# Optimization experiments

Hardware: AMD Instinct MI355X
Metric: run time of the kernel (lower is better)

The kernel has to match this reference:

```python
import jax, jax.numpy as jnp
import numpy as np

D_MODEL = 2048
NUM_HEADS = 32
NUM_KV_HEADS = 8
HEAD_DIM = D_MODEL // NUM_HEADS  # 64
GROUP = NUM_HEADS // NUM_KV_HEADS  # 4


def setup_inputs() -> dict:
    key = jax.random.key(0)
    ks = jax.random.split(key, 9)
    s = 1.0 / np.sqrt(D_MODEL)
    kv_dim = NUM_KV_HEADS * HEAD_DIM
    return {
        "x": jax.random.normal(ks[0], (2, 2048, D_MODEL), dtype=jnp.float32),
        "Wq": jax.random.normal(ks[1], (D_MODEL, D_MODEL), dtype=jnp.float32) * s,
        "bq": jnp.zeros((D_MODEL,), dtype=jnp.float32),
        "Wk": jax.random.normal(ks[2], (D_MODEL, kv_dim), dtype=jnp.float32) * s,
        "bk": jnp.zeros((kv_dim,), dtype=jnp.float32),
        "Wv": jax.random.normal(ks[3], (D_MODEL, kv_dim), dtype=jnp.float32) * s,
        "bv": jnp.zeros((kv_dim,), dtype=jnp.float32),
        "Wo": jax.random.normal(ks[4], (D_MODEL, D_MODEL), dtype=jnp.float32) * s,
        "bo": jnp.zeros((D_MODEL,), dtype=jnp.float32),
    }


def reference(x, Wq, bq, Wk, bk, Wv, bv, Wo, bo):
    B, S, _ = x.shape
    # projections
    q = (x @ Wq + bq).reshape(B, S, NUM_HEADS, HEAD_DIM).transpose(0, 2, 1, 3)      # [B,H,S,Dh]
    k = (x @ Wk + bk).reshape(B, S, NUM_KV_HEADS, HEAD_DIM).transpose(0, 2, 1, 3)   # [B,Hkv,S,Dh]
    v = (x @ Wv + bv).reshape(B, S, NUM_KV_HEADS, HEAD_DIM).transpose(0, 2, 1, 3)
    # expand KV heads to match query heads (repeat_interleave along head dim)
    k = jnp.repeat(k, GROUP, axis=1)  # [B,H,S,Dh]
    v = jnp.repeat(v, GROUP, axis=1)
    scale = 1.0 / np.sqrt(HEAD_DIM).astype(np.float32)
    scores = jnp.einsum('bhqd,bhkd->bhqk', q, k) * scale  # [B,H,S,S]
    attn = jax.nn.softmax(scores, axis=-1)
    out = jnp.einsum('bhqk,bhkd->bhqd', attn, v)          # [B,H,S,Dh]
    out = out.transpose(0, 2, 1, 3).reshape(B, S, NUM_HEADS * HEAD_DIM)
    return out @ Wo + bo
```

## Files before the change

kernel.cpp:

```cpp
#include <hip/hip_runtime.h>
#include <stdint.h>

typedef unsigned short u16;
typedef unsigned int u32;
typedef short bf16x8 __attribute__((ext_vector_type(8)));
typedef float f32x4 __attribute__((ext_vector_type(4)));
typedef u32 u32x2 __attribute__((ext_vector_type(2)));

#define GLOAD_LDS16(gptr, lptr)                                                \
  __builtin_amdgcn_global_load_lds(                                            \
      (__attribute__((address_space(1))) void*)(gptr),                         \
      (__attribute__((address_space(3))) void*)(lptr), 16, 0, 0)

#define WAITV4() asm volatile("s_waitcnt vmcnt(4)" ::: "memory")
#define WAITV0() asm volatile("s_waitcnt vmcnt(0)" ::: "memory")

#if __has_builtin(__builtin_amdgcn_exp2f)
#define EXP2F(x) __builtin_amdgcn_exp2f(x)
#else
#define EXP2F(x) exp2f(x)
#endif

__device__ __forceinline__ u16 f2bf(float f) {
  union { float f; uint32_t u; } v; v.f = f;
  return (u16)((v.u + 0x7fffu + ((v.u >> 16) & 1u)) >> 16);
}
__device__ __forceinline__ float bf2f(u16 h) {
  union { uint32_t u; float f; } v; v.u = ((uint32_t)h) << 16;
  return v.f;
}
__device__ __forceinline__ u32 cvt_pk_bf16(float lo, float hi) {
  u32 r;
  asm("v_cvt_pk_bf16_f32 %0, %1, %2" : "=v"(r) : "v"(lo), "v"(hi));
  return r;
}

__global__ void k_conv_bf16(const float* __restrict__ src, u16* __restrict__ dst, int n8) {
  int i = blockIdx.x * blockDim.x + threadIdx.x;
  if (i >= n8) return;
  const float4* s = (const float4*)src + (size_t)i * 2;
  float4 a = s[0], b = s[1];
  uint4 o;
  o.x = (uint32_t)f2bf(a.x) | ((uint32_t)f2bf(a.y) << 16);
  o.y = (uint32_t)f2bf(a.z) | ((uint32_t)f2bf(a.w) << 16);
  o.z = (uint32_t)f2bf(b.x) | ((uint32_t)f2bf(b.y) << 16);
  o.w = (uint32_t)f2bf(b.z) | ((uint32_t)f2bf(b.w) << 16);
  ((uint4*)dst)[i] = o;
}

__global__ void k_transpose_bf16(const float* __restrict__ src, u16* __restrict__ dst,
                                 int R, int C) {
  __shared__ float tile[32][33];
  int cb = blockIdx.x * 32, rb = blockIdx.y * 32;
  int tx = threadIdx.x, ty = threadIdx.y;
#pragma unroll
  for (int j = 0; j < 4; ++j)
    tile[ty + j * 8][tx] = src[(size_t)(rb + ty + j * 8) * C + cb + tx];
  __syncthreads();
#pragma unroll
  for (int j = 0; j < 4; ++j)
    dst[(size_t)(cb + ty + j * 8) * R + rb + tx] = f2bf(tile[tx][ty + j * 8]);
}

__global__ void k_transpose_v(const u16* __restrict__ cqkv, u16* __restrict__ vt) {
  __shared__ u16 tile[32][34];
  int st = blockIdx.x, dt = blockIdx.y, bk = blockIdx.z;
  int b = bk >> 3, kvh = bk & 7;
  int tx = threadIdx.x, ty = threadIdx.y;
  const u16* src = cqkv + (size_t)(b * 2048 + st * 32) * 3072 + 2560 + kvh * 64 + dt * 32;
#pragma unroll
  for (int j = 0; j < 4; ++j)
    tile[ty + j * 8][tx] = src[(size_t)(ty + j * 8) * 3072 + tx];
  __syncthreads();
  u16* dst = vt + ((size_t)(bk * 64 + dt * 32)) * 2048 + st * 32;
#pragma unroll
  for (int j = 0; j < 4; ++j)
    dst[(size_t)(ty + j * 8) * 2048 + tx] = tile[tx][ty + j * 8];
}

template <bool BF16OUT>
__global__ __launch_bounds__(256) void k_gemm_bt(
    const u16* __restrict__ A, const u16* __restrict__ Bt,
    const float* __restrict__ bias, void* __restrict__ Cptr,
    int M, int N, int K, int gx, int nwg) {
  __shared__ u16 As[3][128 * 32];
  __shared__ u16 Bs[3][128 * 32];
  const int t = threadIdx.x;
  const int lane = t & 63;
  const int w = t >> 6, wr = w >> 1, wc = w & 1;
  const int bid = blockIdx.x;
  const int cpx = nwg >> 3;
  const int swz = (bid & 7) * cpx + (bid >> 3);
  const int brow = (swz / gx) * 128, bcol = (swz % gx) * 128;
  const int g = lane >> 4, q = lane & 15;

  f32x4 acc[4][4] = {};
  const int srow = t >> 2;
  const int sj = t & 3;
  const int jx = sj ^ ((srow >> 1) & 3);
  const int nkt = K >> 5;

  const u16* gA = A + (size_t)(brow + srow) * K + jx * 8;
  const u16* gB = Bt + (size_t)(bcol + srow) * K + jx * 8;

  auto stage = [&](int bb) {
    GLOAD_LDS16(gA,                     (char*)(&As[bb][0]) + t * 16);
    GLOAD_LDS16(gA + (size_t)64 * K,    (char*)(&As[bb][0]) + 4096 + t * 16);
    GLOAD_LDS16(gB,                     (char*)(&Bs[bb][0]) + t * 16);
    GLOAD_LDS16(gB + (size_t)64 * K,    (char*)(&Bs[bb][0]) + 4096 + t * 16);
    gA += 32; gB += 32;
  };

  stage(0);
  stage(1);
  WAITV4();
  __builtin_amdgcn_s_barrier();
  __builtin_amdgcn_sched_barrier(0);

  int cur = 0;
  for (int kt = 0; kt < nkt; ++kt) {
    const u16* Ac = As[cur];
    const u16* Bc = Bs[cur];
    bf16x8 a[4], b[4];
#pragma unroll
    for (int mt = 0; mt < 4; ++mt) {
      int row = wr * 64 + mt * 16 + q;
      int pos = g ^ ((row >> 1) & 3);
      a[mt] = *(const bf16x8*)(Ac + row * 32 + pos * 8);
    }
#pragma unroll
    for (int nt = 0; nt < 4; ++nt) {
      int row = wc * 64 + nt * 16 + q;
      int pos = g ^ ((row >> 1) & 3);
      b[nt] = *(const bf16x8*)(Bc + row * 32 + pos * 8);
    }
    if (kt + 2 < nkt) {
      int b2 = cur + 2; if (b2 >= 3) b2 -= 3;
      stage(b2);
    }
    __builtin_amdgcn_s_setprio(1);
#pragma unroll
    for (int mt = 0; mt < 4; ++mt)
#pragma unroll
      for (int nt = 0; nt < 4; ++nt)
        acc[mt][nt] = __builtin_amdgcn_mfma_f32_16x16x32_bf16(a[mt], b[nt], acc[mt][nt], 0, 0, 0);
    __builtin_amdgcn_s_setprio(0);
    if (kt + 1 < nkt) {
      if (kt + 2 < nkt) WAITV4(); else WAITV0();
      __builtin_amdgcn_s_barrier();
      __builtin_amdgcn_sched_barrier(0);
    }
    ++cur; if (cur >= 3) cur -= 3;
  }
#pragma unroll
  for (int nt = 0; nt < 4; ++nt) {
    int col = bcol + wc * 64 + nt * 16 + q;
    float bv_ = bias[col];
#pragma unroll
    for (int mt = 0; mt < 4; ++mt) {
#pragma unroll
      for (int r = 0; r < 4; ++r) {
        int row = brow + wr * 64 + mt * 16 + g * 4 + r;
        float val = acc[mt][nt][r] + bv_;
        if (BF16OUT)
          ((u16*)Cptr)[(size_t)row * N + col] = f2bf(val);
        else
          ((float*)Cptr)[(size_t)row * N + col] = val;
      }
    }
  }
}

#define LOG2E 1.44269504088896340736f
__global__ __launch_bounds__(256) void k_attn(const u16* __restrict__ qkv,
                                              const u16* __restrict__ vt,
                                              u16* __restrict__ out) {
  const int qt = blockIdx.x, h = blockIdx.y, b = blockIdx.z;
  const int kvh = h >> 2;
  const int t = threadIdx.x, lane = t & 63, w = t >> 6;
  const int g = lane >> 4, q16 = lane & 15;
  const int LDQ = 3072;

  __shared__ u16 Ksh[3][64 * 64];
  __shared__ u16 Vsh[3][64 * 64];
  __shared__ u16 Psh[4][16 * 72] __attribute__((aligned(16)));

  bf16x8 qf[4][2];
#pragma unroll
  for (int s = 0; s < 4; ++s) {
    const size_t qrow = (size_t)(b * 2048 + qt * 256 + s * 64 + w * 16 + q16);
#pragma unroll
    for (int c = 0; c < 2; ++c) {
      bf16x8 tmp = *(const bf16x8*)(qkv + qrow * LDQ + h * 64 + c * 32 + g * 8);
#pragma unroll
      for (int i = 0; i < 8; ++i)
        tmp[i] = (short)f2bf(bf2f((u16)tmp[i]) * 0.125f);
      qf[s][c] = tmp;
    }
  }

  f32x4 acc[4][4] = {};
  float m_run[4], l_run[4];
#pragma unroll
  for (int s = 0; s < 4; ++s) { m_run[s] = -__builtin_inff(); l_run[s] = 0.f; }

  const int kbase = b * 2048;
  const int koff = 2048 + kvh * 64;
  const u16* vtb = vt + (size_t)((b * 8 + kvh) * 64) * 2048;
  const int srow = t >> 3;
  const int sj = t & 7;
  const int cx = sj ^ (srow & 7);

  const u16* gk = qkv + (size_t)(kbase + srow) * LDQ + koff + cx * 8;
  const u16* gv = vtb + (size_t)srow * 2048 + cx * 8;

  auto stage = [&](int bb) {
    GLOAD_LDS16(gk,               (char*)(&Ksh[bb][0]) + t * 16);
    GLOAD_LDS16(gk + 32 * LDQ,    (char*)(&Ksh[bb][0]) + 4096 + t * 16);
    GLOAD_LDS16(gv,               (char*)(&Vsh[bb][0]) + t * 16);
    GLOAD_LDS16(gv + 32 * 2048,   (char*)(&Vsh[bb][0]) + 4096 + t * 16);
    gk += 64 * LDQ; gv += 64;
  };

  stage(0);
  stage(1);
  WAITV4();
  __builtin_amdgcn_s_barrier();
  __builtin_amdgcn_sched_barrier(0);

  int cur = 0;
  for (int kt = 0; kt < 32; ++kt) {
    if (kt + 2 < 32) {
      int b2 = cur + 2; if (b2 >= 3) b2 -= 3;
      stage(b2);
    }
    const u16* Kc = Ksh[cur];
    const u16* Vc = Vsh[cur];

#pragma unroll
    for (int p2 = 0; p2 < 2; ++p2) {
      const int s0 = p2 * 2, s1 = p2 * 2 + 1;
      f32x4 sc[2][4] = {};
      __builtin_amdgcn_s_setprio(1);
#pragma unroll
      for (int c = 0; c < 2; ++c) {
#pragma unroll
        for (int nt = 0; nt < 4; ++nt) {
          int row = nt * 16 + q16;
          bf16x8 kf = *(const bf16x8*)(Kc + row * 64 + (((c * 4 + g) ^ (row & 7)) << 3));
          sc[0][nt] = __builtin_amdgcn_mfma_f32_16x16x32_bf16(kf, qf[s0][c], sc[0][nt], 0, 0, 0);
          sc[1][nt] = __builtin_amdgcn_mfma_f32_16x16x32_bf16(kf, qf[s1][c], sc[1][nt], 0, 0, 0);
        }
      }
      __builtin_amdgcn_s_setprio(0);

      bf16x8 pf[2][2];
#pragma unroll
      for (int i2 = 0; i2 < 2; ++i2) {
        const int s = p2 * 2 + i2;
        float mt_ = sc[i2][0][0];
#pragma unroll
        for (int nt = 0; nt < 4; ++nt)
#pragma unroll
          for (int r = 0; r < 4; ++r)
            mt_ = fmaxf(mt_, sc[i2][nt][r]);
        mt_ = fmaxf(mt_, __shfl_xor(mt_, 16, 64));
        mt_ = fmaxf(mt_, __shfl_xor(mt_, 32, 64));
        if (__any(mt_ > m_run[s])) {
          float mn = fmaxf(m_run[s], mt_);
          float alpha = EXP2F((m_run[s] - mn) * LOG2E);
          m_run[s] = mn;
          l_run[s] *= alpha;
#pragma unroll
          for (int r = 0; r < 4; ++r) {
            float ar = __shfl(alpha, g * 4 + r, 64);
#pragma unroll
            for (int dt = 0; dt < 4; ++dt) acc[s][dt][r] *= ar;
          }
        }
        float mL = m_run[s] * LOG2E;
        float lt = 0.f;
#pragma unroll
        for (int nt = 0; nt < 4; ++nt)
#pragma unroll
          for (int r = 0; r < 4; ++r) {
            float p_ = EXP2F(fmaf(sc[i2][nt][r], LOG2E, -mL));
            sc[i2][nt][r] = p_;
            lt += p_;
          }
        lt += __shfl_xor(lt, 16, 64);
        lt += __shfl_xor(lt, 32, 64);
        l_run[s] += lt;
        u16* prow = &Psh[w][q16 * 72];
#pragma unroll
        for (int nt = 0; nt < 4; ++nt) {
          u32x2 pk;
          pk.x = cvt_pk_bf16(sc[i2][nt][0], sc[i2][nt][1]);
          pk.y = cvt_pk_bf16(sc[i2][nt][2], sc[i2][nt][3]);
          *(u32x2*)(prow + nt * 16 + g * 4) = pk;
        }
        pf[i2][0] = *(const bf16x8*)(&Psh[w][q16 * 72 + g * 8]);
        pf[i2][1] = *(const bf16x8*)(&Psh[w][q16 * 72 + 32 + g * 8]);
      }

      __builtin_amdgcn_s_setprio(1);
#pragma unroll
      for (int c = 0; c < 2; ++c) {
        int kc = c * 4 + g;
#pragma unroll
        for (int dt = 0; dt < 4; ++dt) {
          int d = dt * 16 + q16;
          bf16x8 vf = *(const bf16x8*)(Vc + d * 64 + ((kc ^ (d & 7)) << 3));
          acc[s0][dt] = __builtin_amdgcn_mfma_f32_16x16x32_bf16(pf[0][c], vf, acc[s0][dt], 0, 0, 0);
          acc[s1][dt] = __builtin_amdgcn_mfma_f32_16x16x32_bf16(pf[1][c], vf, acc[s1][dt], 0, 0, 0);
        }
      }
      __builtin_amdgcn_s_setprio(0);
    }

    if (kt + 1 < 32) {
      if (kt + 2 < 32) WAITV4(); else WAITV0();
      __builtin_amdgcn_s_barrier();
      __builtin_amdgcn_sched_barrier(0);
    }
    ++cur; if (cur >= 3) cur -= 3;
  }

#pragma unroll
  for (int s = 0; s < 4; ++s)
#pragma unroll
    for (int r = 0; r < 4; ++r) {
      float linv = 1.0f / __shfl(l_run[s], g * 4 + r, 64);
      size_t orow = (size_t)(b * 2048 + qt * 256 + s * 64 + w * 16 + g * 4 + r);
#pragma unroll
      for (int dt = 0; dt < 4; ++dt)
        out[orow * 2048 + h * 64 + dt * 16 + q16] = f2bf(acc[s][dt][r] * linv);
    }
}

extern "C" void kernel_launch(void* const* d_in, const int* in_sizes, int n_in,
                              void* d_out, int out_size, void* d_ws, size_t ws_size,
                              hipStream_t stream) {
  const float* x  = (const float*)d_in[0];
  const float* Wq = (const float*)d_in[1];
  const float* bq = (const float*)d_in[2];
  const float* Wk = (const float*)d_in[3];
  const float* bk = (const float*)d_in[4];
  const float* Wv = (const float*)d_in[5];
  const float* bv = (const float*)d_in[6];
  const float* Wo = (const float*)d_in[7];
  const float* bo = (const float*)d_in[8];
  float* out = (float*)d_out;

  char* ws = (char*)d_ws;
  u16*   xb    = (u16*)(ws + 0);
  u16*   wqkvT = (u16*)(ws + 16777216);
  u16*   woT   = (u16*)(ws + 29360128);
  float* bqkv  = (float*)(ws + 37748736);
  u16*   cqkv  = (u16*)(ws + 37761024);
  u16*   aout  = (u16*)(ws + 62926848);
  u16*   vtb   = xb;
  (void)ws_size; (void)in_sizes; (void)n_in; (void)out_size;

  hipMemcpyAsync(bqkv, bq, 2048 * sizeof(float), hipMemcpyDeviceToDevice, stream);
  hipMemcpyAsync(bqkv + 2048, bk, 512 * sizeof(float), hipMemcpyDeviceToDevice, stream);
  hipMemcpyAsync(bqkv + 2560, bv, 512 * sizeof(float), hipMemcpyDeviceToDevice, stream);

  k_conv_bf16<<<4096, 256, 0, stream>>>(x, xb, 1048576);
  dim3 tb(32, 8);
  k_transpose_bf16<<<dim3(64, 64), tb, 0, stream>>>(Wq, wqkvT, 2048, 2048);
  k_transpose_bf16<<<dim3(16, 64), tb, 0, stream>>>(Wk, wqkvT + 2048 * 2048, 2048, 512);
  k_transpose_bf16<<<dim3(16, 64), tb, 0, stream>>>(Wv, wqkvT + 2560 * 2048, 2048, 512);
  k_transpose_bf16<<<dim3(64, 64), tb, 0, stream>>>(Wo, woT, 2048, 2048);

  k_gemm_bt<true><<<768, 256, 0, stream>>>(xb, wqkvT, bqkv, cqkv, 4096, 3072, 2048, 24, 768);
  k_transpose_v<<<dim3(64, 2, 16), tb, 0, stream>>>(cqkv, vtb);
  k_attn<<<dim3(8, 32, 2), 256, 0, stream>>>(cqkv, vtb, aout);
  k_gemm_bt<false><<<512, 256, 0, stream>>>(aout, woT, bo, out, 4096, 2048, 2048, 16, 512);
}
```

Baseline: 369.0 us.

## Halve attention query tile, load V straight to registers, double-buffer K

The attention kernel now handles 128 query rows per block instead of 256, which doubles the grid. Each wave loads its V fragments directly from global memory into registers instead of staging V through LDS. K staging drops from triple to double buffering, with plain __syncthreads replacing the vmcnt-based waits. This cuts LDS use and registers per block to allow more blocks in flight, at the cost of less K/V reuse per block and redundant V reads from global/L2 by every wave, with less latency hiding.

```diff
diff --git a/kernel.cpp b/kernel.cpp
--- a/kernel.cpp
+++ b/kernel.cpp
@@ -104,10 +104,10 @@
   const u16* gB = Bt + (size_t)(bcol + srow) * K + jx * 8;
 
   auto stage = [&](int bb) {
-    GLOAD_LDS16(gA,                     (char*)(&As[bb][0]) + t * 16);
-    GLOAD_LDS16(gA + (size_t)64 * K,    (char*)(&As[bb][0]) + 4096 + t * 16);
-    GLOAD_LDS16(gB,                     (char*)(&Bs[bb][0]) + t * 16);
-    GLOAD_LDS16(gB + (size_t)64 * K,    (char*)(&Bs[bb][0]) + 4096 + t * 16);
+    GLOAD_LDS16(gA,                  (char*)(&As[bb][0]) + t * 16);
+    GLOAD_LDS16(gA + (size_t)64 * K, (char*)(&As[bb][0]) + 4096 + t * 16);
+    GLOAD_LDS16(gB,                  (char*)(&Bs[bb][0]) + t * 16);
+    GLOAD_LDS16(gB + (size_t)64 * K, (char*)(&Bs[bb][0]) + 4096 + t * 16);
     gA += 32; gB += 32;
   };
 
@@ -181,14 +181,13 @@
   const int g = lane >> 4, q16 = lane & 15;
   const int LDQ = 3072;
 
-  __shared__ u16 Ksh[3][64 * 64];
-  __shared__ u16 Vsh[3][64 * 64];
+  __shared__ u16 Ksh[2][64 * 64];
   __shared__ u16 Psh[4][16 * 72] __attribute__((aligned(16)));
 
-  bf16x8 qf[4][2];
-#pragma unroll
-  for (int s = 0; s < 4; ++s) {
-    const size_t qrow = (size_t)(b * 2048 + qt * 256 + s * 64 + w * 16 + q16);
+  bf16x8 qf[2][2];
+#pragma unroll
+  for (int s = 0; s < 2; ++s) {
+    const size_t qrow = (size_t)(b * 2048 + qt * 128 + s * 64 + w * 16 + q16);
 #pragma unroll
     for (int c = 0; c < 2; ++c) {
       bf16x8 tmp = *(const bf16x8*)(qkv + qrow * LDQ + h * 64 + c * 32 + g * 8);
@@ -199,10 +198,10 @@
     }
   }
 
-  f32x4 acc[4][4] = {};
-  float m_run[4], l_run[4];
-#pragma unroll
-  for (int s = 0; s < 4; ++s) { m_run[s] = -__builtin_inff(); l_run[s] = 0.f; }
+  f32x4 acc[2][4] = {};
+  float m_run[2], l_run[2];
+  m_run[0] = m_run[1] = -__builtin_inff();
+  l_run[0] = l_run[1] = 0.f;
 
   const int kbase = b * 2048;
   const int koff = 2048 + kvh * 64;
@@ -212,126 +211,117 @@
   const int cx = sj ^ (srow & 7);
 
   const u16* gk = qkv + (size_t)(kbase + srow) * LDQ + koff + cx * 8;
-  const u16* gv = vtb + (size_t)srow * 2048 + cx * 8;
+  const u16* gvd0 = vtb + (size_t)(0 * 16 + q16) * 2048 + g * 8;
+  const u16* gvd1 = vtb + (size_t)(1 * 16 + q16) * 2048 + g * 8;
+  const u16* gvd2 = vtb + (size_t)(2 * 16 + q16) * 2048 + g * 8;
+  const u16* gvd3 = vtb + (size_t)(3 * 16 + q16) * 2048 + g * 8;
 
   auto stage = [&](int bb) {
-    GLOAD_LDS16(gk,               (char*)(&Ksh[bb][0]) + t * 16);
-    GLOAD_LDS16(gk + 32 * LDQ,    (char*)(&Ksh[bb][0]) + 4096 + t * 16);
-    GLOAD_LDS16(gv,               (char*)(&Vsh[bb][0]) + t * 16);
-    GLOAD_LDS16(gv + 32 * 2048,   (char*)(&Vsh[bb][0]) + 4096 + t * 16);
-    gk += 64 * LDQ; gv += 64;
+    GLOAD_LDS16(gk,            (char*)(&Ksh[bb][0]) + t * 16);
+    GLOAD_LDS16(gk + 32 * LDQ, (char*)(&Ksh[bb][0]) + 4096 + t * 16);
+    gk += 64 * LDQ;
   };
 
   stage(0);
-  stage(1);
-  WAITV4();
-  __builtin_amdgcn_s_barrier();
-  __builtin_amdgcn_sched_barrier(0);
-
+  __syncthreads();
   int cur = 0;
+
   for (int kt = 0; kt < 32; ++kt) {
-    if (kt + 2 < 32) {
-      int b2 = cur + 2; if (b2 >= 3) b2 -= 3;
-      stage(b2);
-    }
+    if (kt < 31) stage(cur ^ 1);
     const u16* Kc = Ksh[cur];
-    const u16* Vc = Vsh[cur];
-
-#pragma unroll
-    for (int p2 = 0; p2 < 2; ++p2) {
-      const int s0 = p2 * 2, s1 = p2 * 2 + 1;
-      f32x4 sc[2][4] = {};
-      __builtin_amdgcn_s_setprio(1);
-#pragma unroll
-      for (int c = 0; c < 2; ++c) {
-#pragma unroll
-        for (int nt = 0; nt < 4; ++nt) {
-          int row = nt * 16 + q16;
-          bf16x8 kf = *(const bf16x8*)(Kc + row * 64 + (((c * 4 + g) ^ (row & 7)) << 3));
-          sc[0][nt] = __builtin_amdgcn_mfma_f32_16x16x32_bf16(kf, qf[s0][c], sc[0][nt], 0, 0, 0);
-          sc[1][nt] = __builtin_amdgcn_mfma_f32_16x16x32_bf16(kf, qf[s1][c], sc[1][nt], 0, 0, 0);
+    bf16x8 vf[2][4];
+#pragma unroll
+    for (int c = 0; c < 2; ++c) {
+      vf[c][0] = *(const bf16x8*)(gvd0 + c * 32);
+      vf[c][1] = *(const bf16x8*)(gvd1 + c * 32);
+      vf[c][2] = *(const bf16x8*)(gvd2 + c * 32);
+      vf[c][3] = *(const bf16x8*)(gvd3 + c * 32);
+    }
+    gvd0 += 64; gvd1 += 64; gvd2 += 64; gvd3 += 64;
+
+    f32x4 sc[2][4] = {};
+    __builtin_amdgcn_s_setprio(1);
+#pragma unroll
+    for (int c = 0; c < 2; ++c) {
+#pragma unroll
+      for (int nt = 0; nt < 4; ++nt) {
+        int row = nt * 16 + q16;
+        bf16x8 kf = *(const bf16x8*)(Kc + row * 64 + (((c * 4 + g) ^ (row & 7)) << 3));
+        sc[0][nt] = __builtin_amdgcn_mfma_f32_16x16x32_bf16(kf, qf[0][c], sc[0][nt], 0, 0, 0);
+        sc[1][nt] = __builtin_amdgcn_mfma_f32_16x16x32_bf16(kf, qf[1][c], sc[1][nt], 0, 0, 0);
+      }
+    }
+    __builtin_amdgcn_s_setprio(0);
+
+    bf16x8 pf[2][2];
+#pragma unroll
+    for (int s = 0; s < 2; ++s) {
+      float mt_ = sc[s][0][0];
+#pragma unroll
+      for (int nt = 0; nt < 4; ++nt)
+#pragma unroll
+        for (int r = 0; r < 4; ++r)
+          mt_ = fmaxf(mt_, sc[s][nt][r]);
+      mt_ = fmaxf(mt_, __shfl_xor(mt_, 16, 64));
+      mt_ = fmaxf(mt_, __shfl_xor(mt_, 32, 64));
+      if (__any(mt_ > m_run[s])) {
+        float mn = fmaxf(m_run[s], mt_);
+        float alpha = EXP2F((m_run[s] - mn) * LOG2E);
+        m_run[s] = mn;
+        l_run[s] *= alpha;
+#pragma unroll
+        for (int r = 0; r < 4; ++r) {
+          float ar = __shfl(alpha, g * 4 + r, 64);
+#pragma unroll
+          for (int dt = 0; dt < 4; ++dt) acc[s][dt][r] *= ar;
         }
       }
-      __builtin_amdgcn_s_setprio(0);
-
-      bf16x8 pf[2][2];
-#pragma unroll
-      for (int i2 = 0; i2 < 2; ++i2) {
-        const int s = p2 * 2 + i2;
-        float mt_ = sc[i2][0][0];
-#pragma unroll
-        for (int nt = 0; nt < 4; ++nt)
-#pragma unroll
-          for (int r = 0; r < 4; ++r)
-            mt_ = fmaxf(mt_, sc[i2][nt][r]);
-        mt_ = fmaxf(mt_, __shfl_xor(mt_, 16, 64));
-        mt_ = fmaxf(mt_, __shfl_xor(mt_, 32, 64));
-        if (__any(mt_ > m_run[s])) {
-          float mn = fmaxf(m_run[s], mt_);
-          float alpha = EXP2F((m_run[s] - mn) * LOG2E);
-          m_run[s] = mn;
-          l_run[s] *= alpha;
-#pragma unroll
-          for (int r = 0; r < 4; ++r) {
-            float ar = __shfl(alpha, g * 4 + r, 64);
-#pragma unroll
-            for (int dt = 0; dt < 4; ++dt) acc[s][dt][r] *= ar;
-          }
+      float mL = m_run[s] * LOG2E;
+      float lt = 0.f;
+#pragma unroll
+      for (int nt = 0; nt < 4; ++nt)
+#pragma unroll
+        for (int r = 0; r < 4; ++r) {
+          float p_ = EXP2F(fmaf(sc[s][nt][r], LOG2E, -mL));
+          sc[s][nt][r] = p_;
+          lt += p_;
         }
-        float mL = m_run[s] * LOG2E;
-        float lt = 0.f;
-#pragma unroll
-        for (int nt = 0; nt < 4; ++nt)
-#pragma unroll
-          for (int r = 0; r < 4; ++r) {
-            float p_ = EXP2F(fmaf(sc[i2][nt][r], LOG2E, -mL));
-            sc[i2][nt][r] = p_;
-            lt += p_;
-          }
-        lt += __shfl_xor(lt, 16, 64);
-        lt += __shfl_xor(lt, 32, 64);
-        l_run[s] += lt;
-        u16* prow = &Psh[w][q16 * 72];
-#pragma unroll
-        for (int nt = 0; nt < 4; ++nt) {
-          u32x2 pk;
-          pk.x = cvt_pk_bf16(sc[i2][nt][0], sc[i2][nt][1]);
-          pk.y = cvt_pk_bf16(sc[i2][nt][2], sc[i2][nt][3]);
-          *(u32x2*)(prow + nt * 16 + g * 4) = pk;
-        }
-        pf[i2][0] = *(const bf16x8*)(&Psh[w][q16 * 72 + g * 8]);
-        pf[i2][1] = *(const bf16x8*)(&Psh[w][q16 * 72 + 32 + g * 8]);
-      }
-
-      __builtin_amdgcn_s_setprio(1);
-#pragma unroll
-      for (int c = 0; c < 2; ++c) {
-        int kc = c * 4 + g;
-#pragma unroll
-        for (int dt = 0; dt < 4; ++dt) {
-          int d = dt * 16 + q16;
-          bf16x8 vf = *(const bf16x8*)(Vc + d * 64 + ((kc ^ (d & 7)) << 3));
-          acc[s0][dt] = __builtin_amdgcn_mfma_f32_16x16x32_bf16(pf[0][c], vf, acc[s0][dt], 0, 0, 0);
-          acc[s1][dt] = __builtin_amdgcn_mfma_f32_16x16x32_bf16(pf[1][c], vf, acc[s1][dt], 0, 0, 0);
-        }
-      }
-      __builtin_amdgcn_s_setprio(0);
-    }
-
-    if (kt + 1 < 32) {
-      if (kt + 2 < 32) WAITV4(); else WAITV0();
-      __builtin_amdgcn_s_barrier();
-      __builtin_amdgcn_sched_barrier(0);
-    }
-    ++cur; if (cur >= 3) cur -= 3;
+      lt += __shfl_xor(lt, 16, 64);
+      lt += __shfl_xor(lt, 32, 64);
+      l_run[s] += lt;
+      u16* prow = &Psh[w][q16 * 72];
+#pragma unroll
+      for (int nt = 0; nt < 4; ++nt) {
+        u32x2 pk;
+        pk.x = cvt_pk_bf16(sc[s][nt][0], sc[s][nt][1]);
+        pk.y = cvt_pk_bf16(sc[s][nt][2], sc[s][nt][3]);
+        *(u32x2*)(prow + nt * 16 + g * 4) = pk;
+      }
+      pf[s][0] = *(const bf16x8*)(&Psh[w][q16 * 72 + g * 8]);
+      pf[s][1] = *(const bf16x8*)(&Psh[w][q16 * 72 + 32 + g * 8]);
+    }
+
+    __builtin_amdgcn_s_setprio(1);
+#pragma unroll
+    for (int c = 0; c < 2; ++c) {
+#pragma unroll
+      for (int dt = 0; dt < 4; ++dt) {
+        acc[0][dt] = __builtin_amdgcn_mfma_f32_16x16x32_bf16(pf[0][c], vf[c][dt], acc[0][dt], 0, 0, 0);
+        acc[1][dt] = __builtin_amdgcn_mfma_f32_16x16x32_bf16(pf[1][c], vf[c][dt], acc[1][dt], 0, 0, 0);
+      }
+    }
+    __builtin_amdgcn_s_setprio(0);
+
+    __syncthreads();
+    cur ^= 1;
   }
 
 #pragma unroll
-  for (int s = 0; s < 4; ++s)
+  for (int s = 0; s < 2; ++s)
 #pragma unroll
     for (int r = 0; r < 4; ++r) {
       float linv = 1.0f / __shfl(l_run[s], g * 4 + r, 64);
-      size_t orow = (size_t)(b * 2048 + qt * 256 + s * 64 + w * 16 + g * 4 + r);
+      size_t orow = (size_t)(b * 2048 + qt * 128 + s * 64 + w * 16 + g * 4 + r);
 #pragma unroll
       for (int dt = 0; dt < 4; ++dt)
         out[orow * 2048 + h * 64 + dt * 16 + q16] = f2bf(acc[s][dt][r] * linv);
@@ -375,6 +365,6 @@
 
   k_gemm_bt<true><<<768, 256, 0, stream>>>(xb, wqkvT, bqkv, cqkv, 4096, 3072, 2048, 24, 768);
   k_transpose_v<<<dim3(64, 2, 16), tb, 0, stream>>>(cqkv, vtb);
-  k_attn<<<dim3(8, 32, 2), 256, 0, stream>>>(cqkv, vtb, aout);
+  k_attn<<<dim3(16, 32, 2), 256, 0, stream>>>(cqkv, vtb, aout);
   k_gemm_bt<false><<<512, 256, 0, stream>>>(aout, woT, bo, out, 4096, 2048, 2048, 16, 512);
 }
```

New measurement: 397.8 us. +7.8%, slower.
